# Performance work log

Hardware: AMD Instinct MI355X
Metric: run time of the kernel (lower is better)

## Reference

```python
import jax, jax.numpy as jnp
import numpy as np

EMBED_DIM = 1024
NUM_HEADS = 16
HEAD_DIM = EMBED_DIM // NUM_HEADS


def setup_inputs() -> dict:
    key = jax.random.key(0)
    kx, kq, kk, kv, ko = jax.random.split(key, 5)
    scale = 1.0 / np.sqrt(EMBED_DIM)
    return {
        "x": jax.random.normal(kx, (4, 2048, EMBED_DIM), dtype=jnp.float32),
        # nn.Linear weights are [out, in]; y = x @ W.T
        "w_q": jax.random.normal(kq, (EMBED_DIM, EMBED_DIM), dtype=jnp.float32) * scale,
        "w_k": jax.random.normal(kk, (EMBED_DIM, EMBED_DIM), dtype=jnp.float32) * scale,
        "w_v": jax.random.normal(kv, (EMBED_DIM, EMBED_DIM), dtype=jnp.float32) * scale,
        "w_o": jax.random.normal(ko, (EMBED_DIM, EMBED_DIM), dtype=jnp.float32) * scale,
    }


def reference(x, w_q, w_k, w_v, w_o):
    b, s, _ = x.shape
    # projections (Linear with no bias: x @ W.T)
    q = (x @ w_q.T).reshape(b, s, NUM_HEADS, HEAD_DIM).transpose(0, 2, 1, 3)
    k = (x @ w_k.T).reshape(b, s, NUM_HEADS, HEAD_DIM).transpose(0, 2, 1, 3)
    v = (x @ w_v.T).reshape(b, s, NUM_HEADS, HEAD_DIM).transpose(0, 2, 1, 3)
    # scores: [b, h, s, s]
    scores = jnp.einsum("bhqd,bhkd->bhqk", q, k) / jnp.sqrt(jnp.float32(HEAD_DIM)).astype(x.dtype)
    attn = jax.nn.softmax(scores, axis=-1)
    out = jnp.einsum("bhqk,bhkd->bhqd", attn, v)  # [b, h, s, d]
    out = out.transpose(0, 2, 1, 3).reshape(b, s, EMBED_DIM)
    return out @ w_o.T
```

## Files before the change

kernel.cpp:

```cpp
#include <hip/hip_runtime.h>
#include <math.h>

#define EMBED 1024
#define NHEAD 16
#define HDIM  64
#define BATCH 4
#define SEQ   2048
#define MROWS (BATCH * SEQ)

typedef __attribute__((ext_vector_type(4))) short short4v;
typedef __attribute__((ext_vector_type(8))) short short8;
typedef __attribute__((ext_vector_type(4))) float floatx4;
typedef __attribute__((ext_vector_type(16))) float floatx16;

#if __has_builtin(__builtin_amdgcn_exp2f)
#define EXP2(x) __builtin_amdgcn_exp2f(x)
#else
#define EXP2(x) exp2f(x)
#endif

__device__ __forceinline__ unsigned short f2bf(float f) {
  unsigned u = __float_as_uint(f);
  u += 0x7fffu + ((u >> 16) & 1u);
  return (unsigned short)(u >> 16);
}

#if __has_builtin(__builtin_amdgcn_cvt_pk_bf16_f32)
__device__ __forceinline__ unsigned pack2bf(float lo, float hi) {
  typedef __attribute__((ext_vector_type(2))) __bf16 bf2;
  union { bf2 b; unsigned u; } c;
  c.b = __builtin_amdgcn_cvt_pk_bf16_f32(lo, hi);
  return c.u;
}
#else
__device__ __forceinline__ unsigned pack2bf(float lo, float hi) {
  return ((__float_as_uint(lo) + 0x8000u) >> 16) |
         ((__float_as_uint(hi) + 0x8000u) & 0xffff0000u);
}
#endif

__device__ __forceinline__ void gl_lds16(const void* g, void* l) {
  __builtin_amdgcn_global_load_lds(
      (const __attribute__((address_space(1))) unsigned int*)g,
      (__attribute__((address_space(3))) unsigned int*)l, 16, 0, 0);
}

__global__ __launch_bounds__(256) void cast_bf16_kernel(
    const float* __restrict__ x,  const float* __restrict__ wq,
    const float* __restrict__ wk, const float* __restrict__ wv,
    const float* __restrict__ wo,
    unsigned short* __restrict__ xb, unsigned short* __restrict__ wb) {
  const size_t NX = (size_t)MROWS * EMBED;
  size_t i4 = ((size_t)blockIdx.x * 256 + threadIdx.x) * 4;
  const float* src;
  unsigned short* dst;
  size_t off;
  if (i4 < NX) {
    src = x; dst = xb; off = i4;
  } else {
    size_t j = i4 - NX;
    int r = (int)(j >> 20);
    off = j & ((1u << 20) - 1);
    src = (r == 0) ? wq : (r == 1) ? wk : (r == 2) ? wv : wo;
    dst = wb + ((size_t)r << 20);
  }
  float4 v = *(const float4*)(src + off);
  ushort4 o;
  o.x = f2bf(v.x); o.y = f2bf(v.y); o.z = f2bf(v.z); o.w = f2bf(v.w);
  *(ushort4*)(dst + off) = o;
}

__device__ __forceinline__ void gemm_core(
    const unsigned short* __restrict__ Amat,
    const unsigned short* __restrict__ Bmat,
    int mBase, int nBase,
    unsigned short* As, unsigned short* Bs,
    floatx4 acc[4][4]) {
  const int t = threadIdx.x;
  const int lane = t & 63, w = t >> 6;
  const int wr = w >> 1, wc = w & 1;
  const int quad = lane >> 4, l15 = lane & 15;

  const int f0 = (w * 2 + 0) * 64 + lane;
  const int f1 = (w * 2 + 1) * 64 + lane;
  const unsigned short* ga0 = Amat + (size_t)(mBase + (f0 >> 2)) * EMBED + (f0 & 3) * 8;
  const unsigned short* ga1 = Amat + (size_t)(mBase + (f1 >> 2)) * EMBED + (f1 & 3) * 8;
  const unsigned short* gb0 = Bmat + (size_t)(nBase + (f0 >> 2)) * EMBED + (f0 & 3) * 8;
  const unsigned short* gb1 = Bmat + (size_t)(nBase + (f1 >> 2)) * EMBED + (f1 & 3) * 8;
  unsigned short* la0 = As + (w * 2 + 0) * 512;
  unsigned short* la1 = As + (w * 2 + 1) * 512;
  unsigned short* lb0 = Bs + (w * 2 + 0) * 512;
  unsigned short* lb1 = Bs + (w * 2 + 1) * 512;

  for (int kb = 0; kb < EMBED; kb += 32) {
    __syncthreads();
    gl_lds16(ga0 + kb, la0);
    gl_lds16(ga1 + kb, la1);
    gl_lds16(gb0 + kb, lb0);
    gl_lds16(gb1 + kb, lb1);
    __syncthreads();
    short8 a[4], b[4];
#pragma unroll
    for (int mi = 0; mi < 4; ++mi)
      a[mi] = *(const short8*)&As[(wr * 64 + mi * 16 + l15) * 32 + quad * 8];
#pragma unroll
    for (int ni = 0; ni < 4; ++ni)
      b[ni] = *(const short8*)&Bs[(wc * 64 + ni * 16 + l15) * 32 + quad * 8];
#pragma unroll
    for (int mi = 0; mi < 4; ++mi)
#pragma unroll
      for (int ni = 0; ni < 4; ++ni)
        acc[mi][ni] = __builtin_amdgcn_mfma_f32_16x16x32_bf16(
            a[mi], b[ni], acc[mi][ni], 0, 0, 0);
  }
}

__global__ __launch_bounds__(256) void proj_qkv_bf16(
    const unsigned short* __restrict__ xb,
    const unsigned short* __restrict__ wb,
    unsigned short* __restrict__ qkv) {
  const int which = blockIdx.z;
  const unsigned short* W = wb + ((size_t)which << 20);
  const int nBase = blockIdx.x * 128;
  const int mBase = blockIdx.y * 128;

  __shared__ unsigned short As[128 * 32];
  __shared__ unsigned short Bs[128 * 32];

  floatx4 acc[4][4] = {};
  gemm_core(xb, W, mBase, nBase, As, Bs, acc);

  const int t = threadIdx.x;
  const int lane = t & 63, w = t >> 6;
  const int wr = w >> 1, wc = w & 1;
  const int quad = lane >> 4, l15 = lane & 15;

  unsigned short* out = qkv + (size_t)which * MROWS * EMBED;
  if (which < 2) {
    const float scale = (which == 0) ? 0.18033688f : 1.0f;
#pragma unroll
    for (int mi = 0; mi < 4; ++mi)
#pragma unroll
      for (int ni = 0; ni < 4; ++ni) {
        const int n = nBase + wc * 64 + ni * 16 + l15;
        const int h = n >> 6, d = n & 63;
#pragma unroll
        for (int r = 0; r < 4; ++r) {
          const int m = mBase + wr * 64 + mi * 16 + quad * 4 + r;
          const int b = m >> 11, s = m & (SEQ - 1);
          out[(((size_t)(b * NHEAD + h) * SEQ) + s) * HDIM + d] =
              f2bf(acc[mi][ni][r] * scale);
        }
      }
  } else {
#pragma unroll
    for (int mi = 0; mi < 4; ++mi) {
      const int m0 = mBase + wr * 64 + mi * 16 + quad * 4;
      const int b = m0 >> 11, s0 = m0 & (SEQ - 1);
#pragma unroll
      for (int ni = 0; ni < 4; ++ni) {
        const int n = nBase + wc * 64 + ni * 16 + l15;
        const int h = n >> 6, d = n & 63;
        ushort4 pk;
        pk.x = f2bf(acc[mi][ni][0]); pk.y = f2bf(acc[mi][ni][1]);
        pk.z = f2bf(acc[mi][ni][2]); pk.w = f2bf(acc[mi][ni][3]);
        *(ushort4*)&out[((size_t)(b * NHEAD + h) * HDIM + d) * SEQ + s0] = pk;
      }
    }
  }
}

__global__ __launch_bounds__(256) void attn_mfma(
    const unsigned short* __restrict__ qkv,
    unsigned short* __restrict__ aout) {
  const unsigned short* Q = qkv;
  const unsigned short* K = qkv + (size_t)MROWS * EMBED;
  const unsigned short* V = qkv + 2 * (size_t)MROWS * EMBED;

  const int id = blockIdx.x;
  const int xcd = id & 7, slot = id >> 3;
  const int bh = xcd * 8 + (slot >> 4);
  const int qBase = (slot & 15) * 128;

  __shared__ unsigned short Ks[128 * 64];
  __shared__ unsigned short Vs[64 * 128];

  const int t = threadIdx.x;
  const int lane = t & 63, w = t >> 6;
  const int h2 = lane >> 5;
  const int q31 = lane & 31;

  const unsigned short* qrow =
      Q + ((size_t)bh * SEQ + qBase + w * 32 + q31) * HDIM;
  short8 qa[4];
#pragma unroll
  for (int ds = 0; ds < 4; ++ds)
    qa[ds] = *(const short8*)(qrow + ds * 16 + h2 * 8);

  const unsigned short* kbase = K + (size_t)bh * SEQ * HDIM;
  const unsigned short* vbase = V + (size_t)bh * HDIM * SEQ;
  const unsigned short* gk[4];
  const unsigned short* gv[4];
  unsigned short* lk[4];
  unsigned short* lv[4];
#pragma unroll
  for (int i = 0; i < 4; ++i) {
    const int c = (w * 4 + i) * 64 + lane;
    const int krow = c >> 3, kgrp = (c & 7) ^ (krow & 7);
    gk[i] = kbase + (size_t)krow * HDIM + kgrp * 8;
    const int vd = c >> 4, vj = (c & 15) ^ (vd & 15);
    gv[i] = vbase + (size_t)vd * SEQ + vj * 8;
    lk[i] = Ks + (w * 4 + i) * 512;
    lv[i] = Vs + (w * 4 + i) * 512;
  }

  floatx16 ot0 = {}, ot1 = {};
  float lacc = 0.0f;

  for (int kt = 0; kt < SEQ; kt += 128) {
    __syncthreads();
#pragma unroll
    for (int i = 0; i < 4; ++i) {
      gl_lds16(gk[i] + (size_t)kt * HDIM, lk[i]);
      gl_lds16(gv[i] + kt, lv[i]);
    }
    __syncthreads();

#pragma unroll
    for (int sub = 0; sub < 2; ++sub) {
      const int koff = sub * 64;

      floatx16 st0 = {}, st1 = {};
#pragma unroll
      for (int ds = 0; ds < 4; ++ds) {
        const int g = ds * 2 + h2;
        const int k0 = koff + q31;
        short8 ka0 = *(const short8*)&Ks[k0 * 64 + ((g ^ (q31 & 7)) * 8)];
        st0 = __builtin_amdgcn_mfma_f32_32x32x16_bf16(ka0, qa[ds], st0, 0, 0, 0);
        const int k1 = koff + 32 + q31;
        short8 ka1 = *(const short8*)&Ks[k1 * 64 + ((g ^ (q31 & 7)) * 8)];
        st1 = __builtin_amdgcn_mfma_f32_32x32x16_bf16(ka1, qa[ds], st1, 0, 0, 0);
      }

      float e0[16], e1[16];
#pragma unroll
      for (int i = 0; i < 16; ++i) {
        e0[i] = EXP2(st0[i]);
        e1[i] = EXP2(st1[i]);
        lacc += e0[i] + e1[i];
      }
      unsigned pk0[8], pk1[8];
#pragma unroll
      for (int i = 0; i < 8; ++i) {
        pk0[i] = pack2bf(e0[2 * i], e0[2 * i + 1]);
        pk1[i] = pack2bf(e1[2 * i], e1[2 * i + 1]);
      }

#pragma unroll
      for (int s = 0; s < 8; ++s) {
        const unsigned* pk = (s < 4) ? pk0 : pk1;
        const int rg = s & 3;
        union { unsigned u[2]; short4v v; } pb;
        pb.u[0] = pk[2 * rg + 0];
        pb.u[1] = pk[2 * rg + 1];

        const int g = sub * 8 + s;
        const int pos = ((g ^ (q31 & 15)) * 8) + h2 * 4;
        short4v va0 = *(const short4v*)&Vs[q31 * 128 + pos];
        ot0 = __builtin_amdgcn_mfma_f32_32x32x8bf16_1k(va0, pb.v, ot0, 0, 0, 0);
        short4v va1 = *(const short4v*)&Vs[(32 + q31) * 128 + pos];
        ot1 = __builtin_amdgcn_mfma_f32_32x32x8bf16_1k(va1, pb.v, ot1, 0, 0, 0);
      }
    }
  }

  const float tot = lacc + __shfl_xor(lacc, 32);
  const float inv = 1.0f / tot;

  const int b = bh >> 4, hh = bh & 15;
  unsigned short* orow =
      aout + ((size_t)b * SEQ + qBase + w * 32 + q31) * EMBED + hh * HDIM;
#pragma unroll
  for (int rg = 0; rg < 4; ++rg) {
    const int d0 = rg * 8 + h2 * 4;
    ushort4 p0, p1;
    p0.x = f2bf(ot0[4 * rg + 0] * inv); p0.y = f2bf(ot0[4 * rg + 1] * inv);
    p0.z = f2bf(ot0[4 * rg + 2] * inv); p0.w = f2bf(ot0[4 * rg + 3] * inv);
    *(ushort4*)(orow + d0) = p0;
    p1.x = f2bf(ot1[4 * rg + 0] * inv); p1.y = f2bf(ot1[4 * rg + 1] * inv);
    p1.z = f2bf(ot1[4 * rg + 2] * inv); p1.w = f2bf(ot1[4 * rg + 3] * inv);
    *(ushort4*)(orow + 32 + d0) = p1;
  }
}

__global__ __launch_bounds__(256) void out_proj_bf16(
    const unsigned short* __restrict__ aout,
    const unsigned short* __restrict__ wb,
    float* __restrict__ Cout) {
  const int nBase = blockIdx.x * 128;
  const int mBase = blockIdx.y * 128;

  __shared__ unsigned short As[128 * 32];
  __shared__ unsigned short Bs[128 * 32];

  floatx4 acc[4][4] = {};
  gemm_core(aout, wb + ((size_t)3 << 20), mBase, nBase, As, Bs, acc);

  const int t = threadIdx.x;
  const int lane = t & 63, w = t >> 6;
  const int wr = w >> 1, wc = w & 1;
  const int quad = lane >> 4, l15 = lane & 15;

#pragma unroll
  for (int mi = 0; mi < 4; ++mi)
#pragma unroll
    for (int ni = 0; ni < 4; ++ni) {
      const int n = nBase + wc * 64 + ni * 16 + l15;
#pragma unroll
      for (int r = 0; r < 4; ++r) {
        const int m = mBase + wr * 64 + mi * 16 + quad * 4 + r;
        Cout[(size_t)m * EMBED + n] = acc[mi][ni][r];
      }
    }
}

extern "C" void kernel_launch(void* const* d_in, const int* in_sizes, int n_in,
                              void* d_out, int out_size, void* d_ws, size_t ws_size,
                              hipStream_t stream) {
  const float* x  = (const float*)d_in[0];
  const float* wq = (const float*)d_in[1];
  const float* wk = (const float*)d_in[2];
  const float* wv = (const float*)d_in[3];
  const float* wo = (const float*)d_in[4];
  float* out = (float*)d_out;

  char* ws = (char*)d_ws;
  unsigned short* xb   = (unsigned short*)(ws);
  unsigned short* wb   = (unsigned short*)(ws + (16u << 20));
  unsigned short* qkv  = (unsigned short*)(ws + (26u << 20));
  unsigned short* aout = (unsigned short*)(ws + (76u << 20));

  cast_bf16_kernel<<<12288, 256, 0, stream>>>(x, wq, wk, wv, wo, xb, wb);
  proj_qkv_bf16<<<dim3(EMBED / 128, MROWS / 128, 3), 256, 0, stream>>>(xb, wb, qkv);
  attn_mfma<<<1024, 256, 0, stream>>>(qkv, aout);
  out_proj_bf16<<<dim3(EMBED / 128, MROWS / 128), 256, 0, stream>>>(aout, wb, out);
}
```

Baseline: 297.6 us.

## Double-buffer K/V tiles in attention with 512-thread blocks and MFMA priority

Each attention block now has 8 waves covering 256 query rows, which halves the number of K/V tile loads per query. Shared-memory buffers for K and V are doubled so the next tile's global-to-LDS load is issued before computing on the current one, synchronised with a vmcnt wait and a raw barrier. MFMA sections are given raised wave priority, and the exp/pack loop is fused. The costs are more LDS per block, which may lower occupancy, and a redundant wrap-around prefetch on the last iteration.

```diff
diff --git a/kernel.cpp b/kernel.cpp
--- a/kernel.cpp
+++ b/kernel.cpp
@@ -170,7 +170,7 @@
   }
 }
 
-__global__ __launch_bounds__(256) void attn_mfma(
+__global__ __launch_bounds__(512, 4) void attn_mfma(
     const unsigned short* __restrict__ qkv,
     unsigned short* __restrict__ aout) {
   const unsigned short* Q = qkv;
@@ -179,11 +179,11 @@
 
   const int id = blockIdx.x;
   const int xcd = id & 7, slot = id >> 3;
-  const int bh = xcd * 8 + (slot >> 4);
-  const int qBase = (slot & 15) * 128;
-
-  __shared__ unsigned short Ks[128 * 64];
-  __shared__ unsigned short Vs[64 * 128];
+  const int bh = xcd * 8 + (slot >> 3);
+  const int qBase = (slot & 7) * 256;
+
+  __shared__ unsigned short Ks[2 * 128 * 64];
+  __shared__ unsigned short Vs[2 * 64 * 128];
 
   const int t = threadIdx.x;
   const int lane = t & 63, w = t >> 6;
@@ -199,63 +199,77 @@
 
   const unsigned short* kbase = K + (size_t)bh * SEQ * HDIM;
   const unsigned short* vbase = V + (size_t)bh * HDIM * SEQ;
-  const unsigned short* gk[4];
-  const unsigned short* gv[4];
-  unsigned short* lk[4];
-  unsigned short* lv[4];
-#pragma unroll
-  for (int i = 0; i < 4; ++i) {
-    const int c = (w * 4 + i) * 64 + lane;
+  const unsigned short* gk[2];
+  const unsigned short* gv[2];
+  unsigned short* lk[2];
+  unsigned short* lv[2];
+#pragma unroll
+  for (int i = 0; i < 2; ++i) {
+    const int c = i * 512 + t;
     const int krow = c >> 3, kgrp = (c & 7) ^ (krow & 7);
     gk[i] = kbase + (size_t)krow * HDIM + kgrp * 8;
     const int vd = c >> 4, vj = (c & 15) ^ (vd & 15);
     gv[i] = vbase + (size_t)vd * SEQ + vj * 8;
-    lk[i] = Ks + (w * 4 + i) * 512;
-    lv[i] = Vs + (w * 4 + i) * 512;
+    const int cu = i * 512 + w * 64;
+    lk[i] = Ks + cu * 8;
+    lv[i] = Vs + cu * 8;
   }
 
   floatx16 ot0 = {}, ot1 = {};
   float lacc = 0.0f;
 
+#pragma unroll
+  for (int i = 0; i < 2; ++i) {
+    gl_lds16(gk[i], lk[i]);
+    gl_lds16(gv[i], lv[i]);
+  }
+
   for (int kt = 0; kt < SEQ; kt += 128) {
-    __syncthreads();
-#pragma unroll
-    for (int i = 0; i < 4; ++i) {
-      gl_lds16(gk[i] + (size_t)kt * HDIM, lk[i]);
-      gl_lds16(gv[i] + kt, lv[i]);
+    const int cb = (kt >> 7) & 1;
+    const int nb = cb ^ 1;
+    const int nxt = (kt + 128) & (SEQ - 1);
+    const int sOff = nb * 8192;
+#pragma unroll
+    for (int i = 0; i < 2; ++i) {
+      gl_lds16(gk[i] + (size_t)nxt * HDIM, lk[i] + sOff);
+      gl_lds16(gv[i] + nxt, lv[i] + sOff);
     }
-    __syncthreads();
+    __builtin_amdgcn_sched_barrier(0);
+    asm volatile("s_waitcnt vmcnt(4)" ::: "memory");
+    __builtin_amdgcn_s_barrier();
+
+    const int kOff = cb * 8192;
+    const int vOff = cb * 8192;
 
 #pragma unroll
     for (int sub = 0; sub < 2; ++sub) {
       const int koff = sub * 64;
 
       floatx16 st0 = {}, st1 = {};
+      __builtin_amdgcn_s_setprio(1);
 #pragma unroll
       for (int ds = 0; ds < 4; ++ds) {
         const int g = ds * 2 + h2;
         const int k0 = koff + q31;
-        short8 ka0 = *(const short8*)&Ks[k0 * 64 + ((g ^ (q31 & 7)) * 8)];
+        short8 ka0 = *(const short8*)&Ks[kOff + k0 * 64 + ((g ^ (q31 & 7)) * 8)];
         st0 = __builtin_amdgcn_mfma_f32_32x32x16_bf16(ka0, qa[ds], st0, 0, 0, 0);
         const int k1 = koff + 32 + q31;
-        short8 ka1 = *(const short8*)&Ks[k1 * 64 + ((g ^ (q31 & 7)) * 8)];
+        short8 ka1 = *(const short8*)&Ks[kOff + k1 * 64 + ((g ^ (q31 & 7)) * 8)];
         st1 = __builtin_amdgcn_mfma_f32_32x32x16_bf16(ka1, qa[ds], st1, 0, 0, 0);
       }
-
-      float e0[16], e1[16];
-#pragma unroll
-      for (int i = 0; i < 16; ++i) {
-        e0[i] = EXP2(st0[i]);
-        e1[i] = EXP2(st1[i]);
-        lacc += e0[i] + e1[i];
-      }
+      __builtin_amdgcn_s_setprio(0);
+
       unsigned pk0[8], pk1[8];
 #pragma unroll
       for (int i = 0; i < 8; ++i) {
-        pk0[i] = pack2bf(e0[2 * i], e0[2 * i + 1]);
-        pk1[i] = pack2bf(e1[2 * i], e1[2 * i + 1]);
-      }
-
+        float a0 = EXP2(st0[2 * i]), b0 = EXP2(st0[2 * i + 1]);
+        float a1 = EXP2(st1[2 * i]), b1 = EXP2(st1[2 * i + 1]);
+        lacc += (a0 + b0) + (a1 + b1);
+        pk0[i] = pack2bf(a0, b0);
+        pk1[i] = pack2bf(a1, b1);
+      }
+
+      __builtin_amdgcn_s_setprio(1);
 #pragma unroll
       for (int s = 0; s < 8; ++s) {
         const unsigned* pk = (s < 4) ? pk0 : pk1;
@@ -266,13 +280,18 @@
 
         const int g = sub * 8 + s;
         const int pos = ((g ^ (q31 & 15)) * 8) + h2 * 4;
-        short4v va0 = *(const short4v*)&Vs[q31 * 128 + pos];
+        short4v va0 = *(const short4v*)&Vs[vOff + q31 * 128 + pos];
         ot0 = __builtin_amdgcn_mfma_f32_32x32x8bf16_1k(va0, pb.v, ot0, 0, 0, 0);
-        short4v va1 = *(const short4v*)&Vs[(32 + q31) * 128 + pos];
+        short4v va1 = *(const short4v*)&Vs[vOff + (32 + q31) * 128 + pos];
         ot1 = __builtin_amdgcn_mfma_f32_32x32x8bf16_1k(va1, pb.v, ot1, 0, 0, 0);
       }
+      __builtin_amdgcn_s_setprio(0);
     }
-  }
+
+    __builtin_amdgcn_sched_barrier(0);
+    __builtin_amdgcn_s_barrier();
+  }
+  asm volatile("s_waitcnt vmcnt(0)" ::: "memory");
 
   const float tot = lacc + __shfl_xor(lacc, 32);
   const float inv = 1.0f / tot;
@@ -342,6 +361,6 @@
 
   cast_bf16_kernel<<<12288, 256, 0, stream>>>(x, wq, wk, wv, wo, xb, wb);
   proj_qkv_bf16<<<dim3(EMBED / 128, MROWS / 128, 3), 256, 0, stream>>>(xb, wb, qkv);
-  attn_mfma<<<1024, 256, 0, stream>>>(qkv, aout);
+  attn_mfma<<<512, 512, 0, stream>>>(qkv, aout);
   out_proj_bf16<<<dim3(EMBED / 128, MROWS / 128), 256, 0, stream>>>(aout, wb, out);
 }
```

Measured after the change: 305.7 us. 2.7% more time.
